# Kernel optimization log

Hardware: AMD Instinct MI355X
Metric: run time of the kernel (lower is better)

The kernel has to match this reference:

```python
import jax, jax.numpy as jnp
import numpy as np

EPS = 1e-8  # torch F.cosine_similarity eps


def setup_inputs() -> dict:
    key = jax.random.key(0)
    tensor = jax.random.normal(key, (8192, 256), dtype=jnp.float32)
    return {"tensor": tensor}


def reference(tensor):
    # cosine similarity: L2-normalize rows (norm clamped to eps, matching torch), then Gram GEMM
    norms = jnp.linalg.norm(tensor, axis=-1, keepdims=True)  # [N,1]
    x_hat = tensor / jnp.maximum(norms, EPS)                  # [N,D]
    sim = x_hat @ x_hat.T                                     # [N,N] cosine similarity
    # row-normalize adjacency
    row_sum = jnp.sum(sim, axis=1, keepdims=True)             # [N,1]
    adj = sim / row_sum                                       # [N,N]
    # aggregate
    return adj @ tensor                                       # [N,D]
```

## Files before the change

kernel.cpp:

```cpp
#include <hip/hip_runtime.h>

#define N_ROWS 8192
#define DIM 256
#define EPSF 1e-8f

typedef _Float16 f16x8 __attribute__((ext_vector_type(8)));
typedef _Float16 f16x4 __attribute__((ext_vector_type(4)));
typedef float f32x4 __attribute__((ext_vector_type(4)));

__global__ __launch_bounds__(256) void k1_norm_s(const float* __restrict__ T,
                                                 float* __restrict__ inv_norm,
                                                 double* __restrict__ s) {
    __shared__ double sacc[4][DIM];
    const int lane = threadIdx.x & 63;
    const int wave = threadIdx.x >> 6;
    const int gw = blockIdx.x * 4 + wave;
    const int nw = gridDim.x * 4;
    double a0 = 0.0, a1 = 0.0, a2 = 0.0, a3 = 0.0;
    for (int row = gw; row < N_ROWS; row += nw) {
        float4 v = ((const float4*)(T + (size_t)row * DIM))[lane];
        float ss = v.x * v.x + v.y * v.y + v.z * v.z + v.w * v.w;
#pragma unroll
        for (int o = 32; o; o >>= 1) ss += __shfl_down(ss, o);
        ss = __shfl(ss, 0);
        float inv = 1.0f / fmaxf(sqrtf(ss), EPSF);
        if (lane == 0) inv_norm[row] = inv;
        a0 += (double)(v.x * inv);
        a1 += (double)(v.y * inv);
        a2 += (double)(v.z * inv);
        a3 += (double)(v.w * inv);
    }
    sacc[wave][lane * 4 + 0] = a0;
    sacc[wave][lane * 4 + 1] = a1;
    sacc[wave][lane * 4 + 2] = a2;
    sacc[wave][lane * 4 + 3] = a3;
    __syncthreads();
    const int tid = threadIdx.x;
    double t = sacc[0][tid] + sacc[1][tid] + sacc[2][tid] + sacc[3][tid];
    atomicAdd(&s[tid], t);
}

__global__ __launch_bounds__(256) void k2_rowsum(const float* __restrict__ T,
                                                 const float* __restrict__ inv_norm,
                                                 const double* __restrict__ s,
                                                 float* __restrict__ inv_rs) {
    const int lane = threadIdx.x & 63;
    const int wave = threadIdx.x >> 6;
    const int gw = blockIdx.x * 4 + wave;
    const int nw = gridDim.x * 4;
    const double s0 = s[lane * 4 + 0];
    const double s1 = s[lane * 4 + 1];
    const double s2 = s[lane * 4 + 2];
    const double s3 = s[lane * 4 + 3];
    for (int row = gw; row < N_ROWS; row += nw) {
        float4 v = ((const float4*)(T + (size_t)row * DIM))[lane];
        double d = (double)v.x * s0 + (double)v.y * s1 + (double)v.z * s2 + (double)v.w * s3;
#pragma unroll
        for (int o = 32; o; o >>= 1) d += __shfl_down(d, o);
        if (lane == 0)
            inv_rs[row] = (float)(1.0 / (d * (double)inv_norm[row]));
    }
}

__global__ __launch_bounds__(256) void k_gemmM_mfma(const float* __restrict__ T,
                                                    const float* __restrict__ inv_norm,
                                                    float* __restrict__ partials) {
    const int k0 = blockIdx.x * 128;
    const int d0 = blockIdx.y * 128;
    const int i0 = blockIdx.z * 256;
    __shared__ _Float16 As[128][40];
    __shared__ _Float16 Bs[128][40];
    const int tid = threadIdx.x;
    const int l = tid & 63;
    const int w = tid >> 6;
    const int wy = w >> 1, wx = w & 1;
    const int lm = l & 15, lg = l >> 4;
    f32x4 acc[4][4] = {};
    float4 rA[4], rB[4];
    float rI[4];

    auto stage = [&](int ic) {
#pragma unroll
        for (int j = 0; j < 4; ++j) {
            int idx = tid + 256 * j;
            int i = idx & 31;
            int c4 = (idx >> 5) * 4;
            int gi = i0 + ic + i;
            rI[j] = inv_norm[gi];
            const float* rowp = T + (size_t)gi * DIM;
            rA[j] = *(const float4*)(rowp + k0 + c4);
            rB[j] = *(const float4*)(rowp + d0 + c4);
        }
    };
    auto commit = [&]() {
#pragma unroll
        for (int j = 0; j < 4; ++j) {
            int idx = tid + 256 * j;
            int i = idx & 31;
            int c4 = (idx >> 5) * 4;
            float inv = rI[j];
            As[c4 + 0][i] = (_Float16)(rA[j].x * inv);
            As[c4 + 1][i] = (_Float16)(rA[j].y * inv);
            As[c4 + 2][i] = (_Float16)(rA[j].z * inv);
            As[c4 + 3][i] = (_Float16)(rA[j].w * inv);
            Bs[c4 + 0][i] = (_Float16)rB[j].x;
            Bs[c4 + 1][i] = (_Float16)rB[j].y;
            Bs[c4 + 2][i] = (_Float16)rB[j].z;
            Bs[c4 + 3][i] = (_Float16)rB[j].w;
        }
    };
    auto compute = [&]() {
        f16x8 af[4], bf[4];
#pragma unroll
        for (int mt = 0; mt < 4; ++mt)
            af[mt] = *(const f16x8*)&As[wy * 64 + mt * 16 + lm][lg * 8];
#pragma unroll
        for (int nt = 0; nt < 4; ++nt)
            bf[nt] = *(const f16x8*)&Bs[wx * 64 + nt * 16 + lm][lg * 8];
#pragma unroll
        for (int mt = 0; mt < 4; ++mt)
#pragma unroll
            for (int nt = 0; nt < 4; ++nt)
                acc[mt][nt] = __builtin_amdgcn_mfma_f32_16x16x32_f16(
                    af[mt], bf[nt], acc[mt][nt], 0, 0, 0);
    };

    stage(0);
    commit();
    __syncthreads();
    for (int c = 1; c < 8; ++c) {
        stage(c * 32);
        compute();
        __syncthreads();
        commit();
        __syncthreads();
    }
    compute();

    float* pz = partials + (size_t)blockIdx.z * 65536;
#pragma unroll
    for (int mt = 0; mt < 4; ++mt) {
        int km = k0 + wy * 64 + mt * 16 + lg * 4;
#pragma unroll
        for (int nt = 0; nt < 4; ++nt) {
            int dn = d0 + wx * 64 + nt * 16 + lm;
#pragma unroll
            for (int r = 0; r < 4; ++r)
                pz[(size_t)(km + r) * 256 + dn] = acc[mt][nt][r];
        }
    }
}

__global__ __launch_bounds__(256) void k_reduceM(const float* __restrict__ partials,
                                                 _Float16* __restrict__ Mt) {
    const int g = blockIdx.x * 256 + threadIdx.x;
    const int k = g >> 8, d = g & 255;
    const float* p = partials + (size_t)k * 256 + d;
    float a0 = 0.f, a1 = 0.f, a2 = 0.f, a3 = 0.f;
#pragma unroll
    for (int z = 0; z < 32; z += 4) {
        a0 += p[(size_t)(z + 0) * 65536];
        a1 += p[(size_t)(z + 1) * 65536];
        a2 += p[(size_t)(z + 2) * 65536];
        a3 += p[(size_t)(z + 3) * 65536];
    }
    Mt[(size_t)d * 256 + k] = (_Float16)((a0 + a1) + (a2 + a3));
}

__global__ __launch_bounds__(256) void k3_mfma(const float* __restrict__ T,
                                               const float* __restrict__ inv_norm,
                                               const _Float16* __restrict__ Mt,
                                               const float* __restrict__ inv_rs,
                                               float* __restrict__ out) {
    const int i0 = blockIdx.x * 64;
    const int d0 = blockIdx.y * 64;
    __shared__ _Float16 As[64][40];
    __shared__ _Float16 Bs[64][40];
    const int tid = threadIdx.x;
    const int l = tid & 63;
    const int w = tid >> 6;
    const int wy = w >> 1, wx = w & 1;
    const int lm = l & 15, lg = l >> 4;
    f32x4 acc[2][2] = {};
    float4 rA[2];
    float rI[2];
    f16x8 rB;
    const int db = tid >> 2, k8 = (tid & 3) * 8;

    auto stage = [&](int kc) {
#pragma unroll
        for (int j = 0; j < 2; ++j) {
            int idx = tid + 256 * j;
            int ia = idx >> 3;
            int c4 = (idx & 7) * 4;
            int gi = i0 + ia;
            rI[j] = inv_norm[gi];
            rA[j] = *(const float4*)(T + (size_t)gi * DIM + kc + c4);
        }
        rB = *(const f16x8*)(Mt + (size_t)(d0 + db) * 256 + kc + k8);
    };
    auto commit = [&]() {
#pragma unroll
        for (int j = 0; j < 2; ++j) {
            int idx = tid + 256 * j;
            int ia = idx >> 3;
            int c4 = (idx & 7) * 4;
            float inv = rI[j];
            f16x4 h;
            h[0] = (_Float16)(rA[j].x * inv);
            h[1] = (_Float16)(rA[j].y * inv);
            h[2] = (_Float16)(rA[j].z * inv);
            h[3] = (_Float16)(rA[j].w * inv);
            *(f16x4*)&As[ia][c4] = h;
        }
        *(f16x8*)&Bs[db][k8] = rB;
    };
    auto compute = [&]() {
        f16x8 af[2], bf[2];
#pragma unroll
        for (int ti = 0; ti < 2; ++ti)
            af[ti] = *(const f16x8*)&As[wy * 32 + ti * 16 + lm][lg * 8];
#pragma unroll
        for (int tj = 0; tj < 2; ++tj)
            bf[tj] = *(const f16x8*)&Bs[wx * 32 + tj * 16 + lm][lg * 8];
#pragma unroll
        for (int ti = 0; ti < 2; ++ti)
#pragma unroll
            for (int tj = 0; tj < 2; ++tj)
                acc[ti][tj] = __builtin_amdgcn_mfma_f32_16x16x32_f16(
                    af[ti], bf[tj], acc[ti][tj], 0, 0, 0);
    };

    stage(0);
    commit();
    __syncthreads();
    for (int c = 1; c < 8; ++c) {
        stage(c * 32);
        compute();
        __syncthreads();
        commit();
        __syncthreads();
    }
    compute();

#pragma unroll
    for (int ti = 0; ti < 2; ++ti) {
#pragma unroll
        for (int r = 0; r < 4; ++r) {
            int gi = i0 + wy * 32 + ti * 16 + lg * 4 + r;
            float ir = inv_rs[gi];
#pragma unroll
            for (int tj = 0; tj < 2; ++tj)
                out[(size_t)gi * DIM + d0 + wx * 32 + tj * 16 + lm] =
                    acc[ti][tj][r] * ir;
        }
    }
}

extern "C" void kernel_launch(void* const* d_in, const int* in_sizes, int n_in,
                              void* d_out, int out_size, void* d_ws, size_t ws_size,
                              hipStream_t stream) {
    const float* T = (const float*)d_in[0];
    float* out = (float*)d_out;

    char* ws = (char*)d_ws;
    float* inv_norm = (float*)(ws);
    double* s = (double*)(ws + 32768);
    float* inv_rs = (float*)(ws + 34816);
    _Float16* Mt = (_Float16*)(ws + 67584);
    float* partials = (float*)(ws + 198656);

    hipMemsetAsync(s, 0, 256 * sizeof(double), stream);

    k1_norm_s<<<256, 256, 0, stream>>>(T, inv_norm, s);
    k2_rowsum<<<256, 256, 0, stream>>>(T, inv_norm, s, inv_rs);
    k_gemmM_mfma<<<dim3(2, 2, 32), 256, 0, stream>>>(T, inv_norm, partials);
    k_reduceM<<<256, 256, 0, stream>>>(partials, Mt);
    k3_mfma<<<dim3(128, 4), 256, 0, stream>>>(T, inv_norm, Mt, inv_rs, out);
}
```

Baseline: 104.3 us.

## Fuse all stages into one cooperative persistent kernel with grid syncs

Replaces the memset plus five separate launches with a single cooperative kernel of 512 blocks. Grid-wide syncs separate the norm, column-sum, row-sum, M-GEMM, reduction and final GEMM phases. The column-sum reduction now goes through per-block partials instead of a memset, and tiling is changed to 64x64 tiles over 512 blocks. The aim is to remove launch gaps and the memset, at the cost of grid.sync overhead and a fixed grid that may fit the work less well. The old multi-kernel path is kept as a fallback if the cooperative launch fails.

```diff
diff --git a/kernel.cpp b/kernel.cpp
--- a/kernel.cpp
+++ b/kernel.cpp
@@ -1,4 +1,7 @@
 #include <hip/hip_runtime.h>
+#include <hip/hip_cooperative_groups.h>
+
+namespace cg = cooperative_groups;
 
 #define N_ROWS 8192
 #define DIM 256
@@ -7,6 +10,262 @@
 typedef _Float16 f16x8 __attribute__((ext_vector_type(8)));
 typedef _Float16 f16x4 __attribute__((ext_vector_type(4)));
 typedef float f32x4 __attribute__((ext_vector_type(4)));
+
+__global__ __launch_bounds__(256, 2) void mega(
+    const float* __restrict__ T, float* __restrict__ inv_norm,
+    double* __restrict__ s_part, double* __restrict__ s,
+    float* __restrict__ inv_rs, float* __restrict__ partials,
+    _Float16* __restrict__ Mt, float* __restrict__ out)
+{
+    cg::grid_group grid = cg::this_grid();
+    __shared__ double sacc[4][DIM];
+    __shared__ _Float16 As[64][40];
+    __shared__ _Float16 Bs[64][40];
+
+    const int tid = threadIdx.x;
+    const int bid = blockIdx.x;
+    const int lane = tid & 63;
+    const int wave = tid >> 6;
+
+    float inv_keep[4];
+    {
+        double a0 = 0, a1 = 0, a2 = 0, a3 = 0;
+#pragma unroll
+        for (int r = 0; r < 4; ++r) {
+            int row = bid * 16 + wave * 4 + r;
+            float4 v = ((const float4*)(T + (size_t)row * DIM))[lane];
+            float ss = v.x * v.x + v.y * v.y + v.z * v.z + v.w * v.w;
+#pragma unroll
+            for (int o = 32; o; o >>= 1) ss += __shfl_down(ss, o);
+            ss = __shfl(ss, 0);
+            float inv = 1.0f / fmaxf(sqrtf(ss), EPSF);
+            inv_keep[r] = inv;
+            if (lane == 0) inv_norm[row] = inv;
+            a0 += (double)(v.x * inv);
+            a1 += (double)(v.y * inv);
+            a2 += (double)(v.z * inv);
+            a3 += (double)(v.w * inv);
+        }
+        sacc[wave][lane * 4 + 0] = a0;
+        sacc[wave][lane * 4 + 1] = a1;
+        sacc[wave][lane * 4 + 2] = a2;
+        sacc[wave][lane * 4 + 3] = a3;
+        __syncthreads();
+        double t = sacc[0][tid] + sacc[1][tid] + sacc[2][tid] + sacc[3][tid];
+        s_part[(size_t)bid * DIM + tid] = t;
+    }
+    grid.sync();
+
+    if (bid < 32) {
+        int c8 = tid & 7, m = tid >> 3;
+        int c = bid * 8 + c8;
+        double sum = 0.0;
+#pragma unroll
+        for (int q = 0; q < 16; ++q)
+            sum += s_part[(size_t)(m + 32 * q) * DIM + c];
+        ((double*)sacc)[m * 8 + c8] = sum;
+        __syncthreads();
+        if (tid < 8) {
+            double tot = 0.0;
+#pragma unroll
+            for (int mm = 0; mm < 32; ++mm)
+                tot += ((double*)sacc)[mm * 8 + tid];
+            s[bid * 8 + tid] = tot;
+        }
+    }
+    grid.sync();
+
+    {
+        const double s0 = s[lane * 4 + 0], s1 = s[lane * 4 + 1],
+                     s2 = s[lane * 4 + 2], s3 = s[lane * 4 + 3];
+#pragma unroll
+        for (int r = 0; r < 4; ++r) {
+            int row = bid * 16 + wave * 4 + r;
+            float4 v = ((const float4*)(T + (size_t)row * DIM))[lane];
+            double d = (double)v.x * s0 + (double)v.y * s1 +
+                       (double)v.z * s2 + (double)v.w * s3;
+#pragma unroll
+            for (int o = 32; o; o >>= 1) d += __shfl_down(d, o);
+            if (lane == 0)
+                inv_rs[row] = (float)(1.0 / (d * (double)inv_keep[r]));
+        }
+    }
+
+    {
+        const int kx = bid & 3, dy = (bid >> 2) & 3, z = bid >> 4;
+        const int k0 = kx * 64, d0 = dy * 64, i0 = z * 256;
+        const int wy = wave >> 1, wx = wave & 1;
+        const int lm = lane & 15, lg = lane >> 4;
+        const int i = tid & 31, c8 = tid >> 5;
+        f32x4 acc[2][2] = {};
+        float4 rA[2], rB[2];
+        float rI;
+
+        auto stage = [&](int ic) {
+            int gi = i0 + ic + i;
+            rI = inv_norm[gi];
+            const float* rowp = T + (size_t)gi * DIM;
+#pragma unroll
+            for (int j = 0; j < 2; ++j) {
+                int c4 = (c8 + 8 * j) * 4;
+                rA[j] = *(const float4*)(rowp + k0 + c4);
+                rB[j] = *(const float4*)(rowp + d0 + c4);
+            }
+        };
+        auto commit = [&]() {
+#pragma unroll
+            for (int j = 0; j < 2; ++j) {
+                int c4 = (c8 + 8 * j) * 4;
+                As[c4 + 0][i] = (_Float16)(rA[j].x * rI);
+                As[c4 + 1][i] = (_Float16)(rA[j].y * rI);
+                As[c4 + 2][i] = (_Float16)(rA[j].z * rI);
+                As[c4 + 3][i] = (_Float16)(rA[j].w * rI);
+                Bs[c4 + 0][i] = (_Float16)rB[j].x;
+                Bs[c4 + 1][i] = (_Float16)rB[j].y;
+                Bs[c4 + 2][i] = (_Float16)rB[j].z;
+                Bs[c4 + 3][i] = (_Float16)rB[j].w;
+            }
+        };
+        auto compute = [&]() {
+            f16x8 af[2], bf[2];
+#pragma unroll
+            for (int mt = 0; mt < 2; ++mt)
+                af[mt] = *(const f16x8*)&As[wy * 32 + mt * 16 + lm][lg * 8];
+#pragma unroll
+            for (int nt = 0; nt < 2; ++nt)
+                bf[nt] = *(const f16x8*)&Bs[wx * 32 + nt * 16 + lm][lg * 8];
+#pragma unroll
+            for (int mt = 0; mt < 2; ++mt)
+#pragma unroll
+                for (int nt = 0; nt < 2; ++nt)
+                    acc[mt][nt] = __builtin_amdgcn_mfma_f32_16x16x32_f16(
+                        af[mt], bf[nt], acc[mt][nt], 0, 0, 0);
+        };
+
+        stage(0);
+        commit();
+        __syncthreads();
+        for (int c = 1; c < 8; ++c) {
+            stage(c * 32);
+            compute();
+            __syncthreads();
+            commit();
+            __syncthreads();
+        }
+        compute();
+
+        float* pz = partials + (size_t)z * 65536;
+#pragma unroll
+        for (int mt = 0; mt < 2; ++mt) {
+            int km = k0 + wy * 32 + mt * 16 + lg * 4;
+#pragma unroll
+            for (int nt = 0; nt < 2; ++nt) {
+                int dn = d0 + wx * 32 + nt * 16 + lm;
+#pragma unroll
+                for (int r = 0; r < 4; ++r)
+                    pz[(size_t)(km + r) * 256 + dn] = acc[mt][nt][r];
+            }
+        }
+    }
+    grid.sync();
+
+    if (bid < 256) {
+        int g = bid * 256 + tid;
+        int k = g >> 8, d = g & 255;
+        const float* p = partials + (size_t)k * 256 + d;
+        float a0 = 0.f, a1 = 0.f, a2 = 0.f, a3 = 0.f;
+#pragma unroll
+        for (int zz = 0; zz < 32; zz += 4) {
+            a0 += p[(size_t)(zz + 0) * 65536];
+            a1 += p[(size_t)(zz + 1) * 65536];
+            a2 += p[(size_t)(zz + 2) * 65536];
+            a3 += p[(size_t)(zz + 3) * 65536];
+        }
+        Mt[(size_t)d * 256 + k] = (_Float16)((a0 + a1) + (a2 + a3));
+    }
+    grid.sync();
+
+    {
+        const int i0 = (bid >> 2) * 64;
+        const int d0 = (bid & 3) * 64;
+        const int wy = wave >> 1, wx = wave & 1;
+        const int lm = lane & 15, lg = lane >> 4;
+        f32x4 acc[2][2] = {};
+        float4 rA[2];
+        float rI2[2];
+        f16x8 rB;
+        const int db = tid >> 2, k8 = (tid & 3) * 8;
+
+        auto stage = [&](int kc) {
+#pragma unroll
+            for (int j = 0; j < 2; ++j) {
+                int idx = tid + 256 * j;
+                int ia = idx >> 3;
+                int c4 = (idx & 7) * 4;
+                int gi = i0 + ia;
+                rI2[j] = inv_norm[gi];
+                rA[j] = *(const float4*)(T + (size_t)gi * DIM + kc + c4);
+            }
+            rB = *(const f16x8*)(Mt + (size_t)(d0 + db) * 256 + kc + k8);
+        };
+        auto commit = [&]() {
+#pragma unroll
+            for (int j = 0; j < 2; ++j) {
+                int idx = tid + 256 * j;
+                int ia = idx >> 3;
+                int c4 = (idx & 7) * 4;
+                float inv = rI2[j];
+                f16x4 h;
+                h[0] = (_Float16)(rA[j].x * inv);
+                h[1] = (_Float16)(rA[j].y * inv);
+                h[2] = (_Float16)(rA[j].z * inv);
+                h[3] = (_Float16)(rA[j].w * inv);
+                *(f16x4*)&As[ia][c4] = h;
+            }
+            *(f16x8*)&Bs[db][k8] = rB;
+        };
+        auto compute = [&]() {
+            f16x8 af[2], bf[2];
+#pragma unroll
+            for (int ti = 0; ti < 2; ++ti)
+                af[ti] = *(const f16x8*)&As[wy * 32 + ti * 16 + lm][lg * 8];
+#pragma unroll
+            for (int tj = 0; tj < 2; ++tj)
+                bf[tj] = *(const f16x8*)&Bs[wx * 32 + tj * 16 + lm][lg * 8];
+#pragma unroll
+            for (int ti = 0; ti < 2; ++ti)
+#pragma unroll
+                for (int tj = 0; tj < 2; ++tj)
+                    acc[ti][tj] = __builtin_amdgcn_mfma_f32_16x16x32_f16(
+                        af[ti], bf[tj], acc[ti][tj], 0, 0, 0);
+        };
+
+        stage(0);
+        commit();
+        __syncthreads();
+        for (int c = 1; c < 8; ++c) {
+            stage(c * 32);
+            compute();
+            __syncthreads();
+            commit();
+            __syncthreads();
+        }
+        compute();
+
+#pragma unroll
+        for (int ti = 0; ti < 2; ++ti) {
+#pragma unroll
+            for (int r = 0; r < 4; ++r) {
+                int gi = i0 + wy * 32 + ti * 16 + lg * 4 + r;
+                float ir = inv_rs[gi];
+#pragma unroll
+                for (int tj = 0; tj < 2; ++tj)
+                    out[(size_t)gi * DIM + d0 + wx * 32 + tj * 16 + lm] =
+                        acc[ti][tj][r] * ir;
+            }
+        }
+    }
+}
 
 __global__ __launch_bounds__(256) void k1_norm_s(const float* __restrict__ T,
                                                  float* __restrict__ inv_norm,
@@ -265,16 +524,22 @@
 
     char* ws = (char*)d_ws;
     float* inv_norm = (float*)(ws);
-    double* s = (double*)(ws + 32768);
-    float* inv_rs = (float*)(ws + 34816);
-    _Float16* Mt = (_Float16*)(ws + 67584);
-    float* partials = (float*)(ws + 198656);
-
-    hipMemsetAsync(s, 0, 256 * sizeof(double), stream);
-
-    k1_norm_s<<<256, 256, 0, stream>>>(T, inv_norm, s);
-    k2_rowsum<<<256, 256, 0, stream>>>(T, inv_norm, s, inv_rs);
-    k_gemmM_mfma<<<dim3(2, 2, 32), 256, 0, stream>>>(T, inv_norm, partials);
-    k_reduceM<<<256, 256, 0, stream>>>(partials, Mt);
-    k3_mfma<<<dim3(128, 4), 256, 0, stream>>>(T, inv_norm, Mt, inv_rs, out);
-}
+    double* s_part = (double*)(ws + 32768);
+    double* s = (double*)(ws + 1081344);
+    float* inv_rs = (float*)(ws + 1083392);
+    _Float16* Mt = (_Float16*)(ws + 1116160);
+    float* partials = (float*)(ws + 1247232);
+
+    void* args[] = {(void*)&T, (void*)&inv_norm, (void*)&s_part, (void*)&s,
+                    (void*)&inv_rs, (void*)&partials, (void*)&Mt, (void*)&out};
+    hipError_t e = hipLaunchCooperativeKernel((const void*)mega, dim3(512),
+                                              dim3(256), args, 0, stream);
+    if (e != hipSuccess) {
+        hipMemsetAsync(s, 0, 256 * sizeof(double), stream);
+        k1_norm_s<<<256, 256, 0, stream>>>(T, inv_norm, s);
+        k2_rowsum<<<256, 256, 0, stream>>>(T, inv_norm, s, inv_rs);
+        k_gemmM_mfma<<<dim3(2, 2, 32), 256, 0, stream>>>(T, inv_norm, partials);
+        k_reduceM<<<256, 256, 0, stream>>>(partials, Mt);
+        k3_mfma<<<dim3(128, 4), 256, 0, stream>>>(T, inv_norm, Mt, inv_rs, out);
+    }
+}
```

New measurement: 301.9 us. +189.4%, slower.

## Merge rowsum into M-GEMM kernel, drop atomics/memset, shrink tiles and double-buffer LDS

Applied to the files above, without the earlier changes.

k1 now writes per-block partial column sums instead of using double atomics, which removes the memset. The rowsum pass is folded into the M-GEMM kernel as 64 extra blocks that first reduce those partials, so one launch disappears. Both MFMA GEMMs use smaller tiles (64x64 for M, 32x64 for the output) to launch more blocks, and double-buffer LDS so each chunk needs one barrier instead of two. The cost is redundant reduction of s_part in each of the 64 rowsum blocks and less data reuse per block.

```diff
diff --git a/kernel.cpp b/kernel.cpp
--- a/kernel.cpp
+++ b/kernel.cpp
@@ -5,19 +5,18 @@
 #define EPSF 1e-8f
 
 typedef _Float16 f16x8 __attribute__((ext_vector_type(8)));
-typedef _Float16 f16x4 __attribute__((ext_vector_type(4)));
 typedef float f32x4 __attribute__((ext_vector_type(4)));
 
-__global__ __launch_bounds__(256) void k1_norm_s(const float* __restrict__ T,
-                                                 float* __restrict__ inv_norm,
-                                                 double* __restrict__ s) {
+__global__ __launch_bounds__(256) void k1_norm(const float* __restrict__ T,
+                                               float* __restrict__ inv_norm,
+                                               double* __restrict__ s_part) {
     __shared__ double sacc[4][DIM];
-    const int lane = threadIdx.x & 63;
-    const int wave = threadIdx.x >> 6;
-    const int gw = blockIdx.x * 4 + wave;
-    const int nw = gridDim.x * 4;
-    double a0 = 0.0, a1 = 0.0, a2 = 0.0, a3 = 0.0;
-    for (int row = gw; row < N_ROWS; row += nw) {
+    const int tid = threadIdx.x, bid = blockIdx.x;
+    const int lane = tid & 63, wave = tid >> 6;
+    double a0 = 0, a1 = 0, a2 = 0, a3 = 0;
+#pragma unroll
+    for (int r = 0; r < 4; ++r) {
+        int row = bid * 16 + wave * 4 + r;
         float4 v = ((const float4*)(T + (size_t)row * DIM))[lane];
         float ss = v.x * v.x + v.y * v.y + v.z * v.z + v.w * v.w;
 #pragma unroll
@@ -35,115 +34,126 @@
     sacc[wave][lane * 4 + 2] = a2;
     sacc[wave][lane * 4 + 3] = a3;
     __syncthreads();
-    const int tid = threadIdx.x;
     double t = sacc[0][tid] + sacc[1][tid] + sacc[2][tid] + sacc[3][tid];
-    atomicAdd(&s[tid], t);
-}
-
-__global__ __launch_bounds__(256) void k2_rowsum(const float* __restrict__ T,
-                                                 const float* __restrict__ inv_norm,
-                                                 const double* __restrict__ s,
-                                                 float* __restrict__ inv_rs) {
-    const int lane = threadIdx.x & 63;
-    const int wave = threadIdx.x >> 6;
-    const int gw = blockIdx.x * 4 + wave;
-    const int nw = gridDim.x * 4;
-    const double s0 = s[lane * 4 + 0];
-    const double s1 = s[lane * 4 + 1];
-    const double s2 = s[lane * 4 + 2];
-    const double s3 = s[lane * 4 + 3];
-    for (int row = gw; row < N_ROWS; row += nw) {
-        float4 v = ((const float4*)(T + (size_t)row * DIM))[lane];
-        double d = (double)v.x * s0 + (double)v.y * s1 + (double)v.z * s2 + (double)v.w * s3;
-#pragma unroll
-        for (int o = 32; o; o >>= 1) d += __shfl_down(d, o);
-        if (lane == 0)
-            inv_rs[row] = (float)(1.0 / (d * (double)inv_norm[row]));
-    }
-}
-
-__global__ __launch_bounds__(256) void k_gemmM_mfma(const float* __restrict__ T,
-                                                    const float* __restrict__ inv_norm,
-                                                    float* __restrict__ partials) {
-    const int k0 = blockIdx.x * 128;
-    const int d0 = blockIdx.y * 128;
-    const int i0 = blockIdx.z * 256;
-    __shared__ _Float16 As[128][40];
-    __shared__ _Float16 Bs[128][40];
-    const int tid = threadIdx.x;
-    const int l = tid & 63;
-    const int w = tid >> 6;
-    const int wy = w >> 1, wx = w & 1;
-    const int lm = l & 15, lg = l >> 4;
-    f32x4 acc[4][4] = {};
-    float4 rA[4], rB[4];
-    float rI[4];
+    s_part[(size_t)bid * DIM + tid] = t;
+}
+
+__global__ __launch_bounds__(256) void k2_gemmM(const float* __restrict__ T,
+                                                const float* __restrict__ inv_norm,
+                                                const double* __restrict__ s_part,
+                                                float* __restrict__ inv_rs,
+                                                float* __restrict__ partials) {
+    __shared__ _Float16 As[2][64][40];
+    __shared__ _Float16 Bs[2][64][40];
+    __shared__ double sred[4][DIM];
+    const int tid = threadIdx.x, bid = blockIdx.x;
+    const int lane = tid & 63, wave = tid >> 6;
+
+    if (bid < 64) {
+        double a0 = 0, a1 = 0, a2 = 0, a3 = 0;
+        for (int b = wave * 128; b < wave * 128 + 128; ++b) {
+            const double* rp = s_part + (size_t)b * DIM;
+            a0 += rp[lane * 4 + 0];
+            a1 += rp[lane * 4 + 1];
+            a2 += rp[lane * 4 + 2];
+            a3 += rp[lane * 4 + 3];
+        }
+        sred[wave][lane * 4 + 0] = a0;
+        sred[wave][lane * 4 + 1] = a1;
+        sred[wave][lane * 4 + 2] = a2;
+        sred[wave][lane * 4 + 3] = a3;
+        __syncthreads();
+        double sc = sred[0][tid] + sred[1][tid] + sred[2][tid] + sred[3][tid];
+        __syncthreads();
+        sred[0][tid] = sc;
+        __syncthreads();
+        const double s0 = sred[0][lane * 4 + 0];
+        const double s1 = sred[0][lane * 4 + 1];
+        const double s2 = sred[0][lane * 4 + 2];
+        const double s3 = sred[0][lane * 4 + 3];
+        const int slot = bid * 4 + wave;
+        for (int k = 0; k < 32; ++k) {
+            int row = slot + 256 * k;
+            float4 v = ((const float4*)(T + (size_t)row * DIM))[lane];
+            double d = (double)v.x * s0 + (double)v.y * s1 +
+                       (double)v.z * s2 + (double)v.w * s3;
+#pragma unroll
+            for (int o = 32; o; o >>= 1) d += __shfl_down(d, o);
+            if (lane == 0)
+                inv_rs[row] = (float)(1.0 / (d * (double)inv_norm[row]));
+        }
+        return;
+    }
+
+    const int g = bid - 64;
+    const int k0 = (g & 3) * 64;
+    const int d0 = ((g >> 2) & 3) * 64;
+    const int i0 = (g >> 4) * 256;
+    const int wy = wave >> 1, wx = wave & 1;
+    const int lm = lane & 15, lg = lane >> 4;
+    const int i = tid & 31, c8 = (tid >> 5) * 8;
+    f32x4 acc[2][2] = {};
+    float4 rA[2], rB[2];
+    float rI;
 
     auto stage = [&](int ic) {
-#pragma unroll
-        for (int j = 0; j < 4; ++j) {
-            int idx = tid + 256 * j;
-            int i = idx & 31;
-            int c4 = (idx >> 5) * 4;
-            int gi = i0 + ic + i;
-            rI[j] = inv_norm[gi];
-            const float* rowp = T + (size_t)gi * DIM;
-            rA[j] = *(const float4*)(rowp + k0 + c4);
-            rB[j] = *(const float4*)(rowp + d0 + c4);
-        }
-    };
-    auto commit = [&]() {
-#pragma unroll
-        for (int j = 0; j < 4; ++j) {
-            int idx = tid + 256 * j;
-            int i = idx & 31;
-            int c4 = (idx >> 5) * 4;
-            float inv = rI[j];
-            As[c4 + 0][i] = (_Float16)(rA[j].x * inv);
-            As[c4 + 1][i] = (_Float16)(rA[j].y * inv);
-            As[c4 + 2][i] = (_Float16)(rA[j].z * inv);
-            As[c4 + 3][i] = (_Float16)(rA[j].w * inv);
-            Bs[c4 + 0][i] = (_Float16)rB[j].x;
-            Bs[c4 + 1][i] = (_Float16)rB[j].y;
-            Bs[c4 + 2][i] = (_Float16)rB[j].z;
-            Bs[c4 + 3][i] = (_Float16)rB[j].w;
-        }
-    };
-    auto compute = [&]() {
-        f16x8 af[4], bf[4];
-#pragma unroll
-        for (int mt = 0; mt < 4; ++mt)
-            af[mt] = *(const f16x8*)&As[wy * 64 + mt * 16 + lm][lg * 8];
-#pragma unroll
-        for (int nt = 0; nt < 4; ++nt)
-            bf[nt] = *(const f16x8*)&Bs[wx * 64 + nt * 16 + lm][lg * 8];
-#pragma unroll
-        for (int mt = 0; mt < 4; ++mt)
-#pragma unroll
-            for (int nt = 0; nt < 4; ++nt)
+        int gi = i0 + ic + i;
+        rI = inv_norm[gi];
+        const float* rowp = T + (size_t)gi * DIM;
+        rA[0] = *(const float4*)(rowp + k0 + c8);
+        rA[1] = *(const float4*)(rowp + k0 + c8 + 4);
+        rB[0] = *(const float4*)(rowp + d0 + c8);
+        rB[1] = *(const float4*)(rowp + d0 + c8 + 4);
+    };
+    auto commit = [&](int buf) {
+#pragma unroll
+        for (int j = 0; j < 2; ++j) {
+            float4 a = rA[j], b = rB[j];
+            int c = c8 + j * 4;
+            As[buf][c + 0][i] = (_Float16)(a.x * rI);
+            As[buf][c + 1][i] = (_Float16)(a.y * rI);
+            As[buf][c + 2][i] = (_Float16)(a.z * rI);
+            As[buf][c + 3][i] = (_Float16)(a.w * rI);
+            Bs[buf][c + 0][i] = (_Float16)b.x;
+            Bs[buf][c + 1][i] = (_Float16)b.y;
+            Bs[buf][c + 2][i] = (_Float16)b.z;
+            Bs[buf][c + 3][i] = (_Float16)b.w;
+        }
+    };
+    auto compute = [&](int buf) {
+        f16x8 af[2], bf[2];
+#pragma unroll
+        for (int mt = 0; mt < 2; ++mt)
+            af[mt] = *(const f16x8*)&As[buf][wy * 32 + mt * 16 + lm][lg * 8];
+#pragma unroll
+        for (int nt = 0; nt < 2; ++nt)
+            bf[nt] = *(const f16x8*)&Bs[buf][wx * 32 + nt * 16 + lm][lg * 8];
+#pragma unroll
+        for (int mt = 0; mt < 2; ++mt)
+#pragma unroll
+            for (int nt = 0; nt < 2; ++nt)
                 acc[mt][nt] = __builtin_amdgcn_mfma_f32_16x16x32_f16(
                     af[mt], bf[nt], acc[mt][nt], 0, 0, 0);
     };
 
     stage(0);
-    commit();
+    commit(0);
     __syncthreads();
     for (int c = 1; c < 8; ++c) {
         stage(c * 32);
-        compute();
-        __syncthreads();
-        commit();
-        __syncthreads();
-    }
-    compute();
-
-    float* pz = partials + (size_t)blockIdx.z * 65536;
-#pragma unroll
-    for (int mt = 0; mt < 4; ++mt) {
-        int km = k0 + wy * 64 + mt * 16 + lg * 4;
-#pragma unroll
-        for (int nt = 0; nt < 4; ++nt) {
-            int dn = d0 + wx * 64 + nt * 16 + lm;
+        compute((c - 1) & 1);
+        commit(c & 1);
+        __syncthreads();
+    }
+    compute(1);
+
+    float* pz = partials + (size_t)(g >> 4) * 65536;
+#pragma unroll
+    for (int mt = 0; mt < 2; ++mt) {
+        int km = k0 + wy * 32 + mt * 16 + lg * 4;
+#pragma unroll
+        for (int nt = 0; nt < 2; ++nt) {
+            int dn = d0 + wx * 32 + nt * 16 + lm;
 #pragma unroll
             for (int r = 0; r < 4; ++r)
                 pz[(size_t)(km + r) * 256 + dn] = acc[mt][nt][r];
@@ -153,8 +163,8 @@
 
 __global__ __launch_bounds__(256) void k_reduceM(const float* __restrict__ partials,
                                                  _Float16* __restrict__ Mt) {
-    const int g = blockIdx.x * 256 + threadIdx.x;
-    const int k = g >> 8, d = g & 255;
+    const int gidx = blockIdx.x * 256 + threadIdx.x;
+    const int k = gidx >> 8, d = gidx & 255;
     const float* p = partials + (size_t)k * 256 + d;
     float a0 = 0.f, a1 = 0.f, a2 = 0.f, a3 = 0.f;
 #pragma unroll
@@ -172,88 +182,58 @@
                                                const _Float16* __restrict__ Mt,
                                                const float* __restrict__ inv_rs,
                                                float* __restrict__ out) {
-    const int i0 = blockIdx.x * 64;
-    const int d0 = blockIdx.y * 64;
-    __shared__ _Float16 As[64][40];
-    __shared__ _Float16 Bs[64][40];
-    const int tid = threadIdx.x;
-    const int l = tid & 63;
-    const int w = tid >> 6;
-    const int wy = w >> 1, wx = w & 1;
-    const int lm = l & 15, lg = l >> 4;
-    f32x4 acc[2][2] = {};
-    float4 rA[2];
-    float rI[2];
+    __shared__ _Float16 As[2][32][40];
+    __shared__ _Float16 Bs[2][64][40];
+    const int tid = threadIdx.x, bid = blockIdx.x;
+    const int lane = tid & 63, wave = tid >> 6;
+    const int i0 = (bid >> 2) * 32;
+    const int d0 = (bid & 3) * 64;
+    const int wy = wave >> 1, wx = wave & 1;
+    const int lm = lane & 15, lg = lane >> 4;
+    f32x4 acc[2] = {};
+    float4 rA;
+    float rI;
     f16x8 rB;
+    const int ia = tid >> 3, c4 = (tid & 7) * 4;
     const int db = tid >> 2, k8 = (tid & 3) * 8;
 
     auto stage = [&](int kc) {
-#pragma unroll
-        for (int j = 0; j < 2; ++j) {
-            int idx = tid + 256 * j;
-            int ia = idx >> 3;
-            int c4 = (idx & 7) * 4;
-            int gi = i0 + ia;
-            rI[j] = inv_norm[gi];
-            rA[j] = *(const float4*)(T + (size_t)gi * DIM + kc + c4);
-        }
+        rI = inv_norm[i0 + ia];
+        rA = *(const float4*)(T + (size_t)(i0 + ia) * DIM + kc + c4);
         rB = *(const f16x8*)(Mt + (size_t)(d0 + db) * 256 + kc + k8);
     };
-    auto commit = [&]() {
-#pragma unroll
-        for (int j = 0; j < 2; ++j) {
-            int idx = tid + 256 * j;
-            int ia = idx >> 3;
-            int c4 = (idx & 7) * 4;
-            float inv = rI[j];
-            f16x4 h;
-            h[0] = (_Float16)(rA[j].x * inv);
-            h[1] = (_Float16)(rA[j].y * inv);
-            h[2] = (_Float16)(rA[j].z * inv);
-            h[3] = (_Float16)(rA[j].w * inv);
-            *(f16x4*)&As[ia][c4] = h;
-        }
-        *(f16x8*)&Bs[db][k8] = rB;
-    };
-    auto compute = [&]() {
-        f16x8 af[2], bf[2];
-#pragma unroll
-        for (int ti = 0; ti < 2; ++ti)
-            af[ti] = *(const f16x8*)&As[wy * 32 + ti * 16 + lm][lg * 8];
-#pragma unroll
-        for (int tj = 0; tj < 2; ++tj)
-            bf[tj] = *(const f16x8*)&Bs[wx * 32 + tj * 16 + lm][lg * 8];
-#pragma unroll
-        for (int ti = 0; ti < 2; ++ti)
-#pragma unroll
-            for (int tj = 0; tj < 2; ++tj)
-                acc[ti][tj] = __builtin_amdgcn_mfma_f32_16x16x32_f16(
-                    af[ti], bf[tj], acc[ti][tj], 0, 0, 0);
+    auto commit = [&](int buf) {
+        As[buf][ia][c4 + 0] = (_Float16)(rA.x * rI);
+        As[buf][ia][c4 + 1] = (_Float16)(rA.y * rI);
+        As[buf][ia][c4 + 2] = (_Float16)(rA.z * rI);
+        As[buf][ia][c4 + 3] = (_Float16)(rA.w * rI);
+        *(f16x8*)&Bs[buf][db][k8] = rB;
+    };
+    auto compute = [&](int buf) {
+        f16x8 af = *(const f16x8*)&As[buf][wy * 16 + lm][lg * 8];
+        f16x8 bf0 = *(const f16x8*)&Bs[buf][wx * 32 + lm][lg * 8];
+        f16x8 bf1 = *(const f16x8*)&Bs[buf][wx * 32 + 16 + lm][lg * 8];
+        acc[0] = __builtin_amdgcn_mfma_f32_16x16x32_f16(af, bf0, acc[0], 0, 0, 0);
+        acc[1] = __builtin_amdgcn_mfma_f32_16x16x32_f16(af, bf1, acc[1], 0, 0, 0);
     };
 
     stage(0);
-    commit();
+    commit(0);
     __syncthreads();
     for (int c = 1; c < 8; ++c) {
         stage(c * 32);
-        compute();
-        __syncthreads();
-        commit();
-        __syncthreads();
-    }
-    compute();
-
-#pragma unroll
-    for (int ti = 0; ti < 2; ++ti) {
-#pragma unroll
-        for (int r = 0; r < 4; ++r) {
-            int gi = i0 + wy * 32 + ti * 16 + lg * 4 + r;
-            float ir = inv_rs[gi];
-#pragma unroll
-            for (int tj = 0; tj < 2; ++tj)
-                out[(size_t)gi * DIM + d0 + wx * 32 + tj * 16 + lm] =
-                    acc[ti][tj][r] * ir;
-        }
+        compute((c - 1) & 1);
+        commit(c & 1);
+        __syncthreads();
+    }
+    compute(1);
+
+#pragma unroll
+    for (int r = 0; r < 4; ++r) {
+        int gi = i0 + wy * 16 + lg * 4 + r;
+        float ir = inv_rs[gi];
+        out[(size_t)gi * DIM + d0 + wx * 32 + lm] = acc[0][r] * ir;
+        out[(size_t)gi * DIM + d0 + wx * 32 + 16 + lm] = acc[1][r] * ir;
     }
 }
 
@@ -265,16 +245,13 @@
 
     char* ws = (char*)d_ws;
     float* inv_norm = (float*)(ws);
-    double* s = (double*)(ws + 32768);
-    float* inv_rs = (float*)(ws + 34816);
-    _Float16* Mt = (_Float16*)(ws + 67584);
-    float* partials = (float*)(ws + 198656);
-
-    hipMemsetAsync(s, 0, 256 * sizeof(double), stream);
-
-    k1_norm_s<<<256, 256, 0, stream>>>(T, inv_norm, s);
-    k2_rowsum<<<256, 256, 0, stream>>>(T, inv_norm, s, inv_rs);
-    k_gemmM_mfma<<<dim3(2, 2, 32), 256, 0, stream>>>(T, inv_norm, partials);
+    double* s_part = (double*)(ws + 32768);
+    float* inv_rs = (float*)(ws + 1081344);
+    _Float16* Mt = (_Float16*)(ws + 1114112);
+    float* partials = (float*)(ws + 1245184);
+
+    k1_norm<<<512, 256, 0, stream>>>(T, inv_norm, s_part);
+    k2_gemmM<<<576, 256, 0, stream>>>(T, inv_norm, s_part, inv_rs, partials);
     k_reduceM<<<256, 256, 0, stream>>>(partials, Mt);
-    k3_mfma<<<dim3(128, 4), 256, 0, stream>>>(T, inv_norm, Mt, inv_rs, out);
-}
+    k3_mfma<<<1024, 256, 0, stream>>>(T, inv_norm, Mt, inv_rs, out);
+}
```

Result: slower. 111.9 us (+7.3%).
